# Optimization experiments

Measured on AMD Instinct MI355X. Metric: run time of the kernel, lower is better.

Reference implementation:

```python
import jax, jax.numpy as jnp
from jax import lax
import numpy as np

NUM_ANCHORS = 3
NUM_CLASSES = 20
IMG_DIM = 416.0
ANCHORS = np.array([[10.0, 13.0], [16.0, 30.0], [33.0, 23.0]], dtype=np.float32)
BN_EPS = 1e-5


def setup_inputs() -> dict:
    key = jax.random.key(0)
    ks = jax.random.split(key, 8)
    B, Cin, G = 16, 256, 52
    Cmid = 2 * Cin
    Cout = NUM_ANCHORS * (NUM_CLASSES + 5)
    # weights scaled down so exp() in the box decode stays numerically tame
    return {
        "x": jax.random.normal(ks[0], (B, Cin, G, G), jnp.float32),
        "conv1_w": jax.random.normal(ks[1], (Cmid, Cin, 3, 3), jnp.float32) * 0.05,
        "bn_gamma": jnp.ones((Cmid,), jnp.float32),
        "bn_beta": jnp.zeros((Cmid,), jnp.float32),
        "bn_mean": jax.random.normal(ks[2], (Cmid,), jnp.float32) * 0.05,
        "bn_var": jax.random.uniform(ks[3], (Cmid,), jnp.float32, 0.5, 1.5),
        "conv2_w": jax.random.normal(ks[4], (Cout, Cmid, 1, 1), jnp.float32) * 0.05,
        "conv2_b": jnp.zeros((Cout,), jnp.float32),
    }


def _conv(x, w, padding):
    return lax.conv_general_dilated(
        x, w, window_strides=(1, 1), padding=padding,
        dimension_numbers=("NCHW", "OIHW", "NCHW"))


def reference(x, conv1_w, bn_gamma, bn_beta, bn_mean, bn_var, conv2_w, conv2_b):
    # BasicConv: conv3x3 (no bias) -> BatchNorm (inference stats) -> LeakyReLU(0.1)
    y = _conv(x, conv1_w, ((1, 1), (1, 1)))
    inv = bn_gamma / jnp.sqrt(bn_var + BN_EPS)
    y = y * inv[None, :, None, None] + (bn_beta - bn_mean * inv)[None, :, None, None]
    y = jnp.where(y > 0, y, 0.1 * y)
    # 1x1 head conv with bias
    y = _conv(y, conv2_w, ((0, 0), (0, 0))) + conv2_b[None, :, None, None]

    B, G = y.shape[0], y.shape[2]
    A, NC = NUM_ANCHORS, NUM_CLASSES
    # [B, A, 5+NC, G, G] -> [B, A, G, G, 5+NC]
    pred = y.reshape(B, A, NC + 5, G, G).transpose(0, 1, 3, 4, 2)

    obj_score = jax.nn.sigmoid(pred[..., 4])        # [B,A,G,G]
    pred_cls = jax.nn.sigmoid(pred[..., 5:])        # [B,A,G,G,NC]

    stride = IMG_DIM / G
    grid = jnp.arange(G, dtype=jnp.float32)
    grid_x = grid[None, None, None, :]              # [1,1,1,G]
    grid_y = grid[None, None, :, None]              # [1,1,G,1]
    scaled = jnp.asarray(ANCHORS) / stride          # [A,2]
    anchor_w = scaled[:, 0].reshape(1, A, 1, 1)
    anchor_h = scaled[:, 1].reshape(1, A, 1, 1)

    # original uses .data (detached) for box decode
    box_in = lax.stop_gradient(pred[..., :4])
    bx = jax.nn.sigmoid(box_in[..., 0]) + grid_x
    by = jax.nn.sigmoid(box_in[..., 1]) + grid_y
    bw = jnp.exp(box_in[..., 2]) * anchor_w
    bh = jnp.exp(box_in[..., 3]) * anchor_h
    pred_boxes = jnp.stack([bx, by, bw, bh], axis=-1) * stride  # [B,A,G,G,4]

    return jnp.concatenate(
        [pred_boxes.reshape(B, -1, 4),
         obj_score.reshape(B, -1, 1),
         pred_cls.reshape(B, -1, NC)], axis=-1)
```

## Files before the change

### kernel.cpp

```cpp
#include <hip/hip_runtime.h>

typedef _Float16 f16;
typedef _Float16 f16x8 __attribute__((ext_vector_type(8)));
typedef _Float16 f16x4 __attribute__((ext_vector_type(4)));
typedef float f32x4 __attribute__((ext_vector_type(4)));

#define GDIM 52
#define GG 2704
#define CIN 256
#define CMID 512
#define COUT 75
#define NIMG 16
#define SPT 192
#define NSPB 15
#define PH 60
#define PW 54

#define AG_OFF 0
#define AG_SZ 49152
#define SLAB_OFF 98304
#define SLAB_SZ 24576

#define VMCNT0 asm volatile("s_waitcnt vmcnt(0)" ::: "memory")

__device__ __forceinline__ float sigmoidf_(float x) {
    return 1.0f / (1.0f + __expf(-x));
}

__device__ __forceinline__ void gload16(const void* g, void* l) {
    __builtin_amdgcn_global_load_lds(
        (const __attribute__((address_space(1))) unsigned int*)g,
        (__attribute__((address_space(3))) unsigned int*)l, 16, 0, 0);
}

__global__ __launch_bounds__(256) void k_zero_border(f16* __restrict__ x16p) {
    int ic = blockIdx.x;
    int tid = threadIdx.x;
    f16x8 z;
#pragma unroll
    for (int k = 0; k < 8; ++k) z[k] = (f16)0;
    for (int j = tid; j < 536; j += 256) {
        int row, col;
        if (j < 432) { int r = j / 54; row = (r == 0) ? 0 : 52 + r; col = j % 54; }
        else { int k = j - 432; row = 1 + (k >> 1); col = (k & 1) * 53; }
        f16* p = x16p + (((size_t)ic * PH + row) * PW + col) * 32;
#pragma unroll
        for (int q = 0; q < 4; ++q) *(f16x8*)(p + q * 8) = z;
    }
}

__global__ __launch_bounds__(256) void k_prep_x(const float* __restrict__ x,
                                                f16* __restrict__ x16p) {
    __shared__ float ls[32][133];
    int hw0 = blockIdx.x * 128, ck = blockIdx.y, img = blockIdx.z;
    int tid = threadIdx.x;
    const float* xb = x + ((size_t)img * CIN + ck * 32) * GG;
#pragma unroll
    for (int i = 0; i < 16; ++i) {
        int idx = tid + i * 256;
        int r = idx >> 7, c = idx & 127;
        int hw = hw0 + c;
        ls[r][c] = (hw < GG) ? xb[(size_t)r * GG + hw] : 0.0f;
    }
    __syncthreads();
    int col = tid >> 1, half = tid & 1;
    int hw = hw0 + col;
    if (hw < GG) {
        int h = hw / GDIM, w = hw % GDIM;
        f16* dst = x16p + ((((size_t)img * 8 + ck) * PH + h + 1) * PW + (w + 1)) * 32 + half * 16;
        f16x8 o0, o1;
#pragma unroll
        for (int j = 0; j < 8; ++j) o0[j] = (f16)ls[half * 16 + j][col];
#pragma unroll
        for (int j = 0; j < 8; ++j) o1[j] = (f16)ls[half * 16 + 8 + j][col];
        *(f16x8*)dst = o0;
        *(f16x8*)(dst + 8) = o1;
    }
}

__global__ __launch_bounds__(256) void k_prep_w(
    const float* __restrict__ w1, const float* __restrict__ w2,
    const float* __restrict__ gamma, const float* __restrict__ beta,
    const float* __restrict__ mean, const float* __restrict__ var,
    f16* __restrict__ w16, f16* __restrict__ w2_16,
    float* __restrict__ bnscale, float* __restrict__ bnshift) {
    int i = blockIdx.x * 256 + threadIdx.x;
    int cl = i & 31;
    int co = (i >> 5) & 511;
    int ckt = i >> 14;
    int ck = ckt & 7, tap = ckt >> 3;
    int ci = ck * 32 + cl;
    w16[i] = (f16)w1[(size_t)co * 2304 + ci * 9 + tap];
    if (i < COUT * CMID) w2_16[i] = (f16)w2[i];
    if (i < CMID) {
        float s = gamma[i] * rsqrtf(var[i] + 1e-5f);
        bnscale[i] = s;
        bnshift[i] = beta[i] - mean[i] * s;
    }
}

#define RD(aa, bb, JJ, TAPC)                                                   \
    do {                                                                       \
        const f16* Ab_ = Ag + (JJ) * 8192;                                     \
        const int TPX_ = (((TAPC) / 3 - 1) * PW + ((TAPC) % 3) - 1) * 8;       \
        aa##0 = *(const f16x8*)(Ab_ + a_lane);                                 \
        aa##1 = *(const f16x8*)(Ab_ + a_lane + 128);                           \
        aa##2 = *(const f16x8*)(Ab_ + a_lane + 256);                           \
        aa##3 = *(const f16x8*)(Ab_ + a_lane + 384);                           \
        bb##0 = *(const f16x8*)(Sb + kgx + roff[0] + TPX_);                    \
        bb##1 = *(const f16x8*)(Sb + kgx + roff[1] + TPX_);                    \
        bb##2 = *(const f16x8*)(Sb + kgx + roff[2] + TPX_);                    \
        bb##3 = *(const f16x8*)(Sb + kgx + roff[3] + TPX_);                    \
        bb##4 = *(const f16x8*)(Sb + kgx + roff[4] + TPX_);                    \
        bb##5 = *(const f16x8*)(Sb + kgx + roff[5] + TPX_);                    \
    } while (0)

#define MM1(aa, bb, NF)                                                        \
    do {                                                                       \
        acc[0][NF] = __builtin_amdgcn_mfma_f32_16x16x32_f16(aa##0, bb##NF, acc[0][NF], 0, 0, 0); \
        acc[1][NF] = __builtin_amdgcn_mfma_f32_16x16x32_f16(aa##1, bb##NF, acc[1][NF], 0, 0, 0); \
        acc[2][NF] = __builtin_amdgcn_mfma_f32_16x16x32_f16(aa##2, bb##NF, acc[2][NF], 0, 0, 0); \
        acc[3][NF] = __builtin_amdgcn_mfma_f32_16x16x32_f16(aa##3, bb##NF, acc[3][NF], 0, 0, 0); \
    } while (0)

#define MM(aa, bb)                                                             \
    do {                                                                       \
        MM1(aa, bb, 0); MM1(aa, bb, 1); MM1(aa, bb, 2);                        \
        MM1(aa, bb, 3); MM1(aa, bb, 4); MM1(aa, bb, 5);                        \
    } while (0)

__global__ __launch_bounds__(512, 2) void k_conv1(
    const f16* __restrict__ x16p, const f16* __restrict__ w16,
    const float* __restrict__ bnscale, const float* __restrict__ bnshift,
    f16* __restrict__ y16) {
    __shared__ __align__(16) char smem[147456];
    int img = blockIdx.x / NSPB, sb = blockIdx.x % NSPB;
    int n0 = sb * SPT;
    int h_lo = n0 / GDIM;
    int half = blockIdx.y;
    int co0 = half * 256;
    int tid = threadIdx.x;
    int lane = tid & 63, wave = tid >> 6;
    int wm = wave >> 1, wn = wave & 1;
    int l15 = lane & 15, kg = lane >> 4;
    int a_lane = kg * 2048 + (wm * 64 + l15) * 8;
    int kgx = kg * 3072;

    int roff[6];
#pragma unroll
    for (int nf = 0; nf < 6; ++nf) {
        int n = n0 + wn * 96 + nf * 16 + l15;
        int nc = n < GG ? n : GG - 1;
        int hh = nc / GDIM, ww = nc % GDIM;
        roff[nf] = ((hh - h_lo + 1) * PW + (ww + 1)) * 8;
    }

    f32x4 acc[4][6];
#pragma unroll
    for (int a = 0; a < 4; ++a)
#pragma unroll
        for (int b = 0; b < 6; ++b) {
            acc[a][b][0] = 0.f; acc[a][b][1] = 0.f;
            acc[a][b][2] = 0.f; acc[a][b][3] = 0.f;
        }

    const f16* xbase = x16p + ((size_t)img * 8 * PH + h_lo) * (PW * 32);
    f16x8 A0_0, A0_1, A0_2, A0_3, B0_0, B0_1, B0_2, B0_3, B0_4, B0_5;
    f16x8 A1_0, A1_1, A1_2, A1_3, B1_0, B1_1, B1_2, B1_3, B1_4, B1_5;

#pragma unroll
    for (int j = 0; j < 3; ++j) {
        const f16* wA = w16 + ((size_t)(j * 8) * 512 + co0) * 32;
        f16* dst = (f16*)(smem + AG_OFF) + j * 8192;
#pragma unroll
        for (int p = 0; p < 2; ++p) {
            int u = p * 512 + tid;
            gload16(wA + (size_t)(u & 255) * 32 + (u >> 8) * 8, dst + (size_t)u * 8);
        }
    }
    {
        f16* sd = (f16*)(smem + SLAB_OFF);
#pragma unroll
        for (int p = 0; p < 3; ++p) {
            int c = p * 512 + tid;
            int s = c / 384, pix = c % 384;
            gload16(xbase + (size_t)pix * 32 + s * 8, sd + (size_t)c * 8);
        }
    }

    for (int ck = 0; ck < 8; ++ck) {
#pragma unroll
        for (int ph = 0; ph < 3; ++ph) {
            const int g = ck * 3 + ph;
            VMCNT0;
            __builtin_amdgcn_s_barrier();
            __builtin_amdgcn_sched_barrier(0);
            if (g < 23) {
                const int ckn = (ph == 2) ? ck + 1 : ck;
                const int phn = (ph == 2) ? 0 : ph + 1;
                f16* dst = (f16*)(smem + AG_OFF + ((g + 1) & 1) * AG_SZ);
#pragma unroll
                for (int j = 0; j < 3; ++j) {
                    const f16* wA =
                        w16 + ((size_t)((phn * 3 + j) * 8 + ckn) * 512 + co0) * 32;
#pragma unroll
                    for (int p = 0; p < 2; ++p) {
                        int u = p * 512 + tid;
                        gload16(wA + (size_t)(u & 255) * 32 + (u >> 8) * 8,
                                dst + (size_t)(j * 8192 + u * 8));
                    }
                }
            }
            if (ph == 1 && ck < 7) {
                const f16* sg = xbase + (size_t)(ck + 1) * (PH * PW * 32);
                f16* sd = (f16*)(smem + SLAB_OFF + ((ck + 1) & 1) * SLAB_SZ);
#pragma unroll
                for (int p = 0; p < 3; ++p) {
                    int c = p * 512 + tid;
                    int s = c / 384, pix = c % 384;
                    gload16(sg + (size_t)pix * 32 + s * 8, sd + (size_t)c * 8);
                }
            }
            const f16* Ag = (const f16*)(smem + AG_OFF + (g & 1) * AG_SZ);
            const f16* Sb = (const f16*)(smem + SLAB_OFF + (ck & 1) * SLAB_SZ);
            RD(A0_, B0_, 0, ph * 3 + 0);
            RD(A1_, B1_, 1, ph * 3 + 1);
            MM(A0_, B0_);
            RD(A0_, B0_, 2, ph * 3 + 2);
            MM(A1_, B1_);
            MM(A0_, B0_);
        }
    }
    VMCNT0;
    __syncthreads();
    f16* tb = (f16*)smem;
#pragma unroll
    for (int mf = 0; mf < 4; ++mf) {
        int cr = wm * 64 + mf * 16 + kg * 4;
        f32x4 sc = *(const f32x4*)(bnscale + co0 + cr);
        f32x4 sh = *(const f32x4*)(bnshift + co0 + cr);
#pragma unroll
        for (int nf = 0; nf < 6; ++nf) {
            int pl = wn * 96 + nf * 16 + l15;
            f16x4 o;
#pragma unroll
            for (int i = 0; i < 4; ++i) {
                float v = acc[mf][nf][i] * sc[i] + sh[i];
                o[i] = (f16)(v > 0.f ? v : 0.1f * v);
            }
            *(f16x4*)(tb + pl * 264 + cr) = o;
        }
    }
    __syncthreads();
    int valid = GG - n0; if (valid > SPT) valid = SPT;
    f16* yb = y16 + (size_t)half * (NIMG * (size_t)GG * 256) + ((size_t)img * GG + n0) * 256;
#pragma unroll
    for (int p = 0; p < 12; ++p) {
        int u = p * 512 + tid, pl = u >> 5, slot = u & 31;
        if (pl < valid)
            *(f16x8*)(yb + (size_t)pl * 256 + slot * 8) =
                *(const f16x8*)(tb + pl * 264 + slot * 8);
    }
}

__global__ __launch_bounds__(256) void k_conv2(
    const f16* __restrict__ y16, const f16* __restrict__ w2_16,
    const float* __restrict__ b2, float* __restrict__ out) {
    __shared__ float ct[128][81];
    int img = blockIdx.x / 22, nb = blockIdx.x % 22;
    int n0 = nb * 128;
    int tid = threadIdx.x;
    int lane = tid & 63, wave = tid >> 6;
    int l15 = lane & 15, kg = lane >> 4;

    f32x4 acc[5][2];
#pragma unroll
    for (int a = 0; a < 5; ++a)
#pragma unroll
        for (int b = 0; b < 2; ++b) {
            acc[a][b][0] = 0.f; acc[a][b][1] = 0.f;
            acc[a][b][2] = 0.f; acc[a][b][3] = 0.f;
        }

    int nn[2];
#pragma unroll
    for (int nf = 0; nf < 2; ++nf) {
        int n = n0 + wave * 32 + nf * 16 + l15;
        nn[nf] = n < GG ? n : GG - 1;
    }
    for (int c0 = 0; c0 < CMID; c0 += 32) {
        const f16* yb = y16 + (size_t)(c0 >> 8) * (NIMG * (size_t)GG * 256) +
                        (size_t)img * GG * 256;
        int c = c0 & 255;
        f16x8 af[5];
#pragma unroll
        for (int mf = 0; mf < 5; ++mf) {
            int co = mf * 16 + l15;
            if (co < COUT)
                af[mf] = *(const f16x8*)(w2_16 + (size_t)co * CMID + c0 + kg * 8);
            else {
#pragma unroll
                for (int k = 0; k < 8; ++k) af[mf][k] = (f16)0;
            }
        }
#pragma unroll
        for (int nf = 0; nf < 2; ++nf) {
            f16x8 bf = *(const f16x8*)(yb + (size_t)nn[nf] * 256 + c + kg * 8);
#pragma unroll
            for (int mf = 0; mf < 5; ++mf)
                acc[mf][nf] = __builtin_amdgcn_mfma_f32_16x16x32_f16(
                    af[mf], bf, acc[mf][nf], 0, 0, 0);
        }
    }
#pragma unroll
    for (int mf = 0; mf < 5; ++mf)
#pragma unroll
        for (int nf = 0; nf < 2; ++nf)
            *(f32x4*)(&ct[wave * 32 + nf * 16 + l15][mf * 16 + kg * 4]) = acc[mf][nf];
    __syncthreads();
    for (int j = tid; j < 384; j += 256) {
        int a = j >> 7, nl = j & 127;
        int n = n0 + nl;
        if (n >= GG) continue;
        const float* t = &ct[nl][a * 25];
        float tv[25];
#pragma unroll
        for (int q = 0; q < 25; ++q) tv[q] = t[q] + b2[a * 25 + q];
        int h = n / GDIM, w = n % GDIM;
        const float AW[3] = {10.f, 16.f, 33.f};
        const float AH[3] = {13.f, 30.f, 23.f};
        float bx = (sigmoidf_(tv[0]) + (float)w) * 8.0f;
        float by = (sigmoidf_(tv[1]) + (float)h) * 8.0f;
        float bw_ = __expf(tv[2]) * AW[a];
        float bh_ = __expf(tv[3]) * AH[a];
        float* o = out + ((size_t)img * 8112 + (size_t)a * GG + n) * 25;
        o[0] = bx; o[1] = by; o[2] = bw_; o[3] = bh_;
        o[4] = sigmoidf_(tv[4]);
#pragma unroll
        for (int q = 0; q < 20; ++q) o[5 + q] = sigmoidf_(tv[5 + q]);
    }
}

extern "C" void kernel_launch(void* const* d_in, const int* in_sizes, int n_in,
                              void* d_out, int out_size, void* d_ws, size_t ws_size,
                              hipStream_t stream) {
    (void)in_sizes; (void)n_in; (void)out_size; (void)ws_size;
    const float* x     = (const float*)d_in[0];
    const float* w1    = (const float*)d_in[1];
    const float* gamma = (const float*)d_in[2];
    const float* beta  = (const float*)d_in[3];
    const float* mean  = (const float*)d_in[4];
    const float* var   = (const float*)d_in[5];
    const float* w2    = (const float*)d_in[6];
    const float* b2    = (const float*)d_in[7];
    float* out = (float*)d_out;

    char* ws = (char*)d_ws;
    f16* x16p     = (f16*)(ws);
    f16* w16      = (f16*)(ws + 26542080);
    f16* w2_16    = (f16*)(ws + 28901376);
    float* bnscale = (float*)(ws + 28978176);
    float* bnshift = (float*)(ws + 28980224);
    f16* y16      = (f16*)(ws + 28982272);

    k_zero_border<<<NIMG * 8, 256, 0, stream>>>(x16p);
    k_prep_x<<<dim3(22, 8, NIMG), 256, 0, stream>>>(x, x16p);
    k_prep_w<<<4608, 256, 0, stream>>>(w1, w2, gamma, beta, mean, var,
                                       w16, w2_16, bnscale, bnshift);
    k_conv1<<<dim3(NIMG * NSPB, 2), 512, 0, stream>>>(x16p, w16, bnscale,
                                                      bnshift, y16);
    k_conv2<<<NIMG * 22, 256, 0, stream>>>(y16, w2_16, b2, out);
}
```

Measured before the change: 161.3 us.

## Load conv1 weight fragments directly from global into registers, bypassing LDS

The 3x3 conv main loop no longer stages weight tiles in double-buffered LDS. Each wave now reads its A fragments straight from global memory into registers, using register double buffering across the nine taps. This cuts barriers from three per channel chunk to one and shrinks the LDS footprint, keeping only the input slab in shared memory. In exchange, waves sharing the same rows duplicate weight loads through cache. It also exposes global-load latency with only one tap of lookahead.

```diff
diff --git a/kernel.cpp b/kernel.cpp
--- a/kernel.cpp
+++ b/kernel.cpp
@@ -16,9 +16,6 @@
 #define PH 60
 #define PW 54
 
-#define AG_OFF 0
-#define AG_SZ 49152
-#define SLAB_OFF 98304
 #define SLAB_SZ 24576
 
 #define VMCNT0 asm volatile("s_waitcnt vmcnt(0)" ::: "memory")
@@ -99,20 +96,25 @@
     }
 }
 
-#define RD(aa, bb, JJ, TAPC)                                                   \
-    do {                                                                       \
-        const f16* Ab_ = Ag + (JJ) * 8192;                                     \
-        const int TPX_ = (((TAPC) / 3 - 1) * PW + ((TAPC) % 3) - 1) * 8;       \
-        aa##0 = *(const f16x8*)(Ab_ + a_lane);                                 \
-        aa##1 = *(const f16x8*)(Ab_ + a_lane + 128);                           \
-        aa##2 = *(const f16x8*)(Ab_ + a_lane + 256);                           \
-        aa##3 = *(const f16x8*)(Ab_ + a_lane + 384);                           \
-        bb##0 = *(const f16x8*)(Sb + kgx + roff[0] + TPX_);                    \
-        bb##1 = *(const f16x8*)(Sb + kgx + roff[1] + TPX_);                    \
-        bb##2 = *(const f16x8*)(Sb + kgx + roff[2] + TPX_);                    \
-        bb##3 = *(const f16x8*)(Sb + kgx + roff[3] + TPX_);                    \
-        bb##4 = *(const f16x8*)(Sb + kgx + roff[4] + TPX_);                    \
-        bb##5 = *(const f16x8*)(Sb + kgx + roff[5] + TPX_);                    \
+#define TPX(T) ((((T) / 3 - 1) * PW + ((T) % 3) - 1) * 8)
+
+#define LDA(aa, TAPN, CKE)                                                     \
+    do {                                                                       \
+        const f16* ap_ = wAfrag + ((size_t)((TAPN) * 8 + (CKE))) * 16384;      \
+        aa##0 = *(const f16x8*)(ap_);                                          \
+        aa##1 = *(const f16x8*)(ap_ + 512);                                    \
+        aa##2 = *(const f16x8*)(ap_ + 1024);                                   \
+        aa##3 = *(const f16x8*)(ap_ + 1536);                                   \
+    } while (0)
+
+#define LDB(bb, TAPC)                                                          \
+    do {                                                                       \
+        bb##0 = *(const f16x8*)(Sb + kgx + roff[0] + TPX(TAPC));               \
+        bb##1 = *(const f16x8*)(Sb + kgx + roff[1] + TPX(TAPC));               \
+        bb##2 = *(const f16x8*)(Sb + kgx + roff[2] + TPX(TAPC));               \
+        bb##3 = *(const f16x8*)(Sb + kgx + roff[3] + TPX(TAPC));               \
+        bb##4 = *(const f16x8*)(Sb + kgx + roff[4] + TPX(TAPC));               \
+        bb##5 = *(const f16x8*)(Sb + kgx + roff[5] + TPX(TAPC));               \
     } while (0)
 
 #define MM1(aa, bb, NF)                                                        \
@@ -129,11 +131,27 @@
         MM1(aa, bb, 3); MM1(aa, bb, 4); MM1(aa, bb, 5);                        \
     } while (0)
 
+#define SB0 __builtin_amdgcn_sched_barrier(0)
+
+#define CKBODY(AC, AN, BC, BN)                                                 \
+    do {                                                                       \
+        LDB(BC, 0); SB0;                                                       \
+        LDA(AN, 1, ck);  LDB(BN, 1); MM(AC, BC); SB0;                          \
+        LDA(AC, 2, ck);  LDB(BC, 2); MM(AN, BN); SB0;                          \
+        LDA(AN, 3, ck);  LDB(BN, 3); MM(AC, BC); SB0;                          \
+        LDA(AC, 4, ck);  LDB(BC, 4); MM(AN, BN); SB0;                          \
+        LDA(AN, 5, ck);  LDB(BN, 5); MM(AC, BC); SB0;                          \
+        LDA(AC, 6, ck);  LDB(BC, 6); MM(AN, BN); SB0;                          \
+        LDA(AN, 7, ck);  LDB(BN, 7); MM(AC, BC); SB0;                          \
+        LDA(AC, 8, ck);  LDB(BC, 8); MM(AN, BN); SB0;                          \
+        LDA(AN, 0, ckn); MM(AC, BC); SB0;                                      \
+    } while (0)
+
 __global__ __launch_bounds__(512, 2) void k_conv1(
     const f16* __restrict__ x16p, const f16* __restrict__ w16,
     const float* __restrict__ bnscale, const float* __restrict__ bnshift,
     f16* __restrict__ y16) {
-    __shared__ __align__(16) char smem[147456];
+    __shared__ __align__(16) char smem[101376];
     int img = blockIdx.x / NSPB, sb = blockIdx.x % NSPB;
     int n0 = sb * SPT;
     int h_lo = n0 / GDIM;
@@ -143,7 +161,6 @@
     int lane = tid & 63, wave = tid >> 6;
     int wm = wave >> 1, wn = wave & 1;
     int l15 = lane & 15, kg = lane >> 4;
-    int a_lane = kg * 2048 + (wm * 64 + l15) * 8;
     int kgx = kg * 3072;
 
     int roff[6];
@@ -165,70 +182,43 @@
         }
 
     const f16* xbase = x16p + ((size_t)img * 8 * PH + h_lo) * (PW * 32);
-    f16x8 A0_0, A0_1, A0_2, A0_3, B0_0, B0_1, B0_2, B0_3, B0_4, B0_5;
-    f16x8 A1_0, A1_1, A1_2, A1_3, B1_0, B1_1, B1_2, B1_3, B1_4, B1_5;
-
-#pragma unroll
-    for (int j = 0; j < 3; ++j) {
-        const f16* wA = w16 + ((size_t)(j * 8) * 512 + co0) * 32;
-        f16* dst = (f16*)(smem + AG_OFF) + j * 8192;
-#pragma unroll
-        for (int p = 0; p < 2; ++p) {
-            int u = p * 512 + tid;
-            gload16(wA + (size_t)(u & 255) * 32 + (u >> 8) * 8, dst + (size_t)u * 8);
-        }
-    }
+    const f16* wAfrag = w16 + (size_t)co0 * 32 + (wm * 64 + l15) * 32 + kg * 8;
+    f16x8 Ae_0, Ae_1, Ae_2, Ae_3, Ao_0, Ao_1, Ao_2, Ao_3;
+    f16x8 Be_0, Be_1, Be_2, Be_3, Be_4, Be_5;
+    f16x8 Bo_0, Bo_1, Bo_2, Bo_3, Bo_4, Bo_5;
+
     {
-        f16* sd = (f16*)(smem + SLAB_OFF);
+        f16* sd = (f16*)smem;
 #pragma unroll
         for (int p = 0; p < 3; ++p) {
             int c = p * 512 + tid;
             int s = c / 384, pix = c % 384;
             gload16(xbase + (size_t)pix * 32 + s * 8, sd + (size_t)c * 8);
         }
+        LDA(Ae_, 0, 0);
     }
 
     for (int ck = 0; ck < 8; ++ck) {
-#pragma unroll
-        for (int ph = 0; ph < 3; ++ph) {
-            const int g = ck * 3 + ph;
-            VMCNT0;
-            __builtin_amdgcn_s_barrier();
-            __builtin_amdgcn_sched_barrier(0);
-            if (g < 23) {
-                const int ckn = (ph == 2) ? ck + 1 : ck;
-                const int phn = (ph == 2) ? 0 : ph + 1;
-                f16* dst = (f16*)(smem + AG_OFF + ((g + 1) & 1) * AG_SZ);
-#pragma unroll
-                for (int j = 0; j < 3; ++j) {
-                    const f16* wA =
-                        w16 + ((size_t)((phn * 3 + j) * 8 + ckn) * 512 + co0) * 32;
-#pragma unroll
-                    for (int p = 0; p < 2; ++p) {
-                        int u = p * 512 + tid;
-                        gload16(wA + (size_t)(u & 255) * 32 + (u >> 8) * 8,
-                                dst + (size_t)(j * 8192 + u * 8));
-                    }
-                }
+        VMCNT0;
+        __builtin_amdgcn_s_barrier();
+        SB0;
+        if (ck < 7) {
+            const f16* sg = xbase + (size_t)(ck + 1) * (PH * PW * 32);
+            f16* sd = (f16*)(smem + ((ck + 1) & 1) * SLAB_SZ);
+#pragma unroll
+            for (int p = 0; p < 3; ++p) {
+                int c = p * 512 + tid;
+                int s = c / 384, pix = c % 384;
+                gload16(sg + (size_t)pix * 32 + s * 8, sd + (size_t)c * 8);
             }
-            if (ph == 1 && ck < 7) {
-                const f16* sg = xbase + (size_t)(ck + 1) * (PH * PW * 32);
-                f16* sd = (f16*)(smem + SLAB_OFF + ((ck + 1) & 1) * SLAB_SZ);
-#pragma unroll
-                for (int p = 0; p < 3; ++p) {
-                    int c = p * 512 + tid;
-                    int s = c / 384, pix = c % 384;
-                    gload16(sg + (size_t)pix * 32 + s * 8, sd + (size_t)c * 8);
-                }
-            }
-            const f16* Ag = (const f16*)(smem + AG_OFF + (g & 1) * AG_SZ);
-            const f16* Sb = (const f16*)(smem + SLAB_OFF + (ck & 1) * SLAB_SZ);
-            RD(A0_, B0_, 0, ph * 3 + 0);
-            RD(A1_, B1_, 1, ph * 3 + 1);
-            MM(A0_, B0_);
-            RD(A0_, B0_, 2, ph * 3 + 2);
-            MM(A1_, B1_);
-            MM(A0_, B0_);
+        }
+        SB0;
+        const f16* Sb = (const f16*)(smem + (ck & 1) * SLAB_SZ);
+        const int ckn = (ck < 7) ? ck + 1 : 7;
+        if (!(ck & 1)) {
+            CKBODY(Ae_, Ao_, Be_, Bo_);
+        } else {
+            CKBODY(Ao_, Ae_, Bo_, Be_);
         }
     }
     VMCNT0;
```

Result: slower. 313.4 us (+94.3%).
